# Kernel optimization log

Hardware: AMD Instinct MI355X
Metric: run time of the kernel (lower is better)

The kernel has to match this reference:

```python
import jax, jax.numpy as jnp
import numpy as np
import math

D = 1024
H = 16

def setup_inputs() -> dict:
    key = jax.random.key(0)
    ks = jax.random.split(key, 8)
    N, X, T = 2, 1024, 4096
    s = 1.0 / math.sqrt(D)
    return {
        "previous_output": jax.random.normal(ks[0], (N, X, D), jnp.float32),
        "context": jax.random.normal(ks[1], (N, T, D), jnp.float32),
        "Wq": jax.random.normal(ks[2], (D, D), jnp.float32) * s,
        "bq": jnp.zeros((D,), jnp.float32),
        "Wk": jax.random.normal(ks[3], (D, D), jnp.float32) * s,
        "bk": jnp.zeros((D,), jnp.float32),
        "Wv": jax.random.normal(ks[4], (D, D), jnp.float32) * s,
        "bv": jnp.zeros((D,), jnp.float32),
    }

def reference(previous_output, context, Wq, bq, Wk, bk, Wv, bv):
    N, X, _ = previous_output.shape
    T = context.shape[1]
    hd = D // H
    # linear projections (torch Linear: x @ W.T + b)
    q = (previous_output @ Wq.T + bq).reshape(N, X, H, hd).transpose(0, 2, 1, 3)  # (N,H,X,hd)
    k = (context @ Wk.T + bk).reshape(N, T, H, hd).transpose(0, 2, 1, 3)          # (N,H,T,hd)
    v = (context @ Wv.T + bv).reshape(N, T, H, hd).transpose(0, 2, 1, 3)          # (N,H,T,hd)
    scores = jnp.einsum('nhxd,nhtd->nhxt', q, k) / jnp.sqrt(jnp.float32(hd))       # (N,H,X,T)
    attn = jax.nn.softmax(scores, axis=-1)
    out = jnp.einsum('nhxt,nhtd->nhxd', attn, v)                                   # (N,H,X,hd)
    return out.transpose(0, 2, 1, 3).reshape(N, X, D)
```

## Files before the change

kernel.cpp:

```cpp
#include <hip/hip_runtime.h>

typedef __bf16 bf16_t;
typedef __bf16 bf16x8 __attribute__((ext_vector_type(8)));
typedef __bf16 bf16x4 __attribute__((ext_vector_type(4)));
typedef float f32x4 __attribute__((ext_vector_type(4)));

#define D_MODEL 1024
#define NHEAD 16
#define HD 64
#define XLEN 1024
#define TLEN 4096
#define NBATCH 2
#define CEXP 0.18033688011112042f

typedef __attribute__((address_space(3))) bf16_t lds_bf16;
typedef const __attribute__((address_space(1))) bf16_t glb_bf16;

#define MEMFENCE() asm volatile("" ::: "memory")

__global__ __launch_bounds__(256) void convert5(const float* __restrict__ prev, const float* __restrict__ ctx,
                                                const float* __restrict__ wq, const float* __restrict__ wk,
                                                const float* __restrict__ wv,
                                                bf16_t* __restrict__ prev_b, bf16_t* __restrict__ ctx_b,
                                                bf16_t* __restrict__ wq_b, bf16_t* __restrict__ wk_b,
                                                bf16_t* __restrict__ wv_b) {
    int b = blockIdx.x;
    const float* src; bf16_t* dst; int lb;
    if (b < 256)       { src = prev; dst = prev_b; lb = b; }
    else if (b < 1280) { src = ctx;  dst = ctx_b;  lb = b - 256; }
    else if (b < 1408) { src = wq;   dst = wq_b;   lb = b - 1280; }
    else if (b < 1536) { src = wk;   dst = wk_b;   lb = b - 1408; }
    else               { src = wv;   dst = wv_b;   lb = b - 1536; }
    const int base = lb * 8192 + threadIdx.x * 4;
#pragma unroll
    for (int i = 0; i < 8; ++i) {
        const int off = base + i * 1024;
        f32x4 f = *(const f32x4*)(src + off);
        bf16x4 h;
        h[0] = (bf16_t)f[0]; h[1] = (bf16_t)f[1]; h[2] = (bf16_t)f[2]; h[3] = (bf16_t)f[3];
        *(bf16x4*)(dst + off) = h;
    }
}

template<int MF>
__device__ __forceinline__ void gemm_core(const bf16_t* __restrict__ Xa,
                                          const bf16_t* __restrict__ Wb,
                                          int m0, int n0, char* smem,
                                          f32x4 (&acc)[MF][4]) {
    const int tid  = threadIdx.x;
    const int w    = tid >> 6;
    const int lane = tid & 63;
    const int q4   = lane >> 4;
    const int c    = lane & 15;
    const int wm   = w >> 2;
    const int wn   = w & 3;

    constexpr int ABYTES = MF * 2048;
    constexpr int BUFSZ  = ABYTES + 16384;
    constexpr int AINSTR = MF / 4;
    constexpr int NT     = 32;

#pragma unroll
    for (int i = 0; i < MF; ++i)
#pragma unroll
        for (int j = 0; j < 4; ++j) acc[i][j] = (f32x4){0.f, 0.f, 0.f, 0.f};

    const int xp = ((lane & 3) * 16) ^ (((lane >> 5) & 1) << 5);
    const char* gA = (const char*)Xa + ((size_t)(m0 + w * 16 + (lane >> 2)) << 11) + xp;
    const char* gB = (const char*)Wb + ((size_t)(n0 + w * 16 + (lane >> 2)) << 11) + xp;
    char* lw = smem + w * 1024;

    const int fo = c * 64 + ((q4 * 16) ^ (((c >> 3) & 1) << 5));

#pragma unroll
    for (int t = 0; t < 3; ++t) {
#pragma unroll
        for (int i = 0; i < AINSTR; ++i)
            __builtin_amdgcn_global_load_lds((glb_bf16*)(gA + (size_t)i * 262144 + t * 64),
                                             (lds_bf16*)(lw + t * BUFSZ + i * 8192), 16, 0, 0);
#pragma unroll
        for (int i = 0; i < 2; ++i)
            __builtin_amdgcn_global_load_lds((glb_bf16*)(gB + (size_t)i * 262144 + t * 64),
                                             (lds_bf16*)(lw + t * BUFSZ + ABYTES + i * 8192), 16, 0, 0);
        MEMFENCE();
    }

#pragma unroll 1
    for (int t = 0; t < NT; ++t) {
        if (t < NT - 2) {
            if constexpr (AINSTR == 2) asm volatile("s_waitcnt vmcnt(8)" ::: "memory");
            else                       asm volatile("s_waitcnt vmcnt(6)" ::: "memory");
        } else if (t == NT - 2) {
            if constexpr (AINSTR == 2) asm volatile("s_waitcnt vmcnt(4)" ::: "memory");
            else                       asm volatile("s_waitcnt vmcnt(3)" ::: "memory");
        } else {
            asm volatile("s_waitcnt vmcnt(0)" ::: "memory");
        }
        __builtin_amdgcn_s_barrier();
        MEMFENCE();

        const char* cbuf = smem + (t & 3) * BUFSZ;
        char* pbuf = lw + ((t + 3) & 3) * BUFSZ;
        const bool pf = (t + 3) < NT;
        const int tk = (t + 3) * 64;

        if (pf) {
#pragma unroll
            for (int i = 0; i < AINSTR; ++i)
                __builtin_amdgcn_global_load_lds((glb_bf16*)(gA + (size_t)i * 262144 + tk),
                                                 (lds_bf16*)(pbuf + i * 8192), 16, 0, 0);
        }
        bf16x8 bfrag[4];
#pragma unroll
        for (int ni = 0; ni < 4; ++ni)
            bfrag[ni] = *(const bf16x8*)(cbuf + ABYTES + (wn * 4 + ni) * 1024 + fo);
        bf16x8 afrag[MF / 2];
#pragma unroll
        for (int mi = 0; mi < MF / 2; ++mi)
            afrag[mi] = *(const bf16x8*)(cbuf + (wm * MF + mi) * 1024 + fo);
        __builtin_amdgcn_s_setprio(1);
#pragma unroll
        for (int mi = 0; mi < MF / 2; ++mi)
#pragma unroll
            for (int ni = 0; ni < 4; ++ni)
                acc[mi][ni] = __builtin_amdgcn_mfma_f32_16x16x32_bf16(afrag[mi], bfrag[ni], acc[mi][ni], 0, 0, 0);
        __builtin_amdgcn_s_setprio(0);
        MEMFENCE();
        __builtin_amdgcn_s_barrier();
        MEMFENCE();

        if (pf) {
#pragma unroll
            for (int i = 0; i < 2; ++i)
                __builtin_amdgcn_global_load_lds((glb_bf16*)(gB + (size_t)i * 262144 + tk),
                                                 (lds_bf16*)(pbuf + ABYTES + i * 8192), 16, 0, 0);
        }
        bf16x8 afrag2[MF / 2];
#pragma unroll
        for (int mi = 0; mi < MF / 2; ++mi)
            afrag2[mi] = *(const bf16x8*)(cbuf + (wm * MF + MF / 2 + mi) * 1024 + fo);
        __builtin_amdgcn_s_setprio(1);
#pragma unroll
        for (int mi = 0; mi < MF / 2; ++mi)
#pragma unroll
            for (int ni = 0; ni < 4; ++ni)
                acc[MF / 2 + mi][ni] = __builtin_amdgcn_mfma_f32_16x16x32_bf16(afrag2[mi], bfrag[ni], acc[MF / 2 + mi][ni], 0, 0, 0);
        __builtin_amdgcn_s_setprio(0);
        MEMFENCE();
    }
}

__global__ __launch_bounds__(512, 2) void gemm_fused2(
    const bf16_t* __restrict__ Xq, const bf16_t* __restrict__ Xc,
    const bf16_t* __restrict__ wq, const bf16_t* __restrict__ wk, const bf16_t* __restrict__ wv,
    const float* __restrict__ bq, const float* __restrict__ bk, const float* __restrict__ bv,
    bf16_t* __restrict__ Qh, bf16_t* __restrict__ Kh, bf16_t* __restrict__ Vt) {
    __shared__ __align__(16) char smem[131072];
    const int bid  = blockIdx.x;
    const int tid  = threadIdx.x;
    const int w    = tid >> 6;
    const int lane = tid & 63;
    const int q4   = lane >> 4;
    const int c    = lane & 15;
    const int wm   = w >> 2;
    const int wn   = w & 3;

    if (bid >= 64) {
        const int b     = bid - 64;
        const int r     = b & 7;
        const int j     = (b >> 3) & 7;
        const int mhi   = b >> 6;
        const int vmode = j >> 2;
        const int n0    = (j & 3) * 256;
        const int m0    = (mhi * 8 + r) * 256;
        const bf16_t* W   = vmode ? wv : wk;
        const float* bias = vmode ? bv : bk;

        const int Nw = n0 + wn * 64;
        float bz[4];
#pragma unroll
        for (int ni = 0; ni < 4; ++ni) bz[ni] = bias[Nw + ni * 16 + c];
        MEMFENCE();

        f32x4 acc[8][4];
        gemm_core<8>(Xc, W, m0, n0, smem, acc);

        const int Mw = m0 + wm * 128;
        const int headbase = Nw >> 6;
        if (vmode == 0) {
#pragma unroll
            for (int mi = 0; mi < 8; ++mi) {
                const int mrow = Mw + mi * 16 + q4 * 4;
                const int nb2 = mrow >> 12, pos = mrow & 4095;
                bf16_t* ob = Kh + ((size_t)(nb2 * NHEAD + headbase) * TLEN + pos) * HD;
#pragma unroll
                for (int ni = 0; ni < 4; ++ni) {
                    const int d = ni * 16 + c;
#pragma unroll
                    for (int r2 = 0; r2 < 4; ++r2)
                        ob[(size_t)r2 * HD + d] = (bf16_t)(acc[mi][ni][r2] + bz[ni]);
                }
            }
        } else {
#pragma unroll
            for (int mi = 0; mi < 8; ++mi) {
                const int mrow = Mw + mi * 16 + q4 * 4;
                const int nb2 = mrow >> 12, pos = mrow & 4095;
                const int lin = (pos & ~31) + ((pos >> 2) & 3) * 8 + ((pos >> 4) & 1) * 4;
#pragma unroll
                for (int ni = 0; ni < 4; ++ni) {
                    const int d = ni * 16 + c;
                    bf16x4 v4;
#pragma unroll
                    for (int r2 = 0; r2 < 4; ++r2) v4[r2] = (bf16_t)(acc[mi][ni][r2] + bz[ni]);
                    *(bf16x4*)(Vt + ((size_t)(nb2 * NHEAD + headbase) * HD + d) * TLEN + lin) = v4;
                }
            }
        }
    } else {
        const int b  = bid;
        const int m0 = (b >> 2) * 128;
        const int n0 = (b & 3) * 256;

        const int Nw = n0 + wn * 64;
        float bz[4];
#pragma unroll
        for (int ni = 0; ni < 4; ++ni) bz[ni] = bq[Nw + ni * 16 + c];
        MEMFENCE();

        f32x4 acc[4][4];
        gemm_core<4>(Xq, wq, m0, n0, smem, acc);

        const int Mw = m0 + wm * 64;
        const int headbase = Nw >> 6;
#pragma unroll
        for (int mi = 0; mi < 4; ++mi) {
            const int mrow = Mw + mi * 16 + q4 * 4;
            const int nb2 = mrow >> 10, pos = mrow & 1023;
            bf16_t* ob = Qh + ((size_t)(nb2 * NHEAD + headbase) * XLEN + pos) * HD;
#pragma unroll
            for (int ni = 0; ni < 4; ++ni) {
                const int d = ni * 16 + c;
#pragma unroll
                for (int r2 = 0; r2 < 4; ++r2)
                    ob[(size_t)r2 * HD + d] = (bf16_t)((acc[mi][ni][r2] + bz[ni]) * CEXP);
            }
        }
    }
}

__global__ __launch_bounds__(256, 4) void attn_kernel(const bf16_t* __restrict__ Qh,
                                                      const bf16_t* __restrict__ Kh,
                                                      const bf16_t* __restrict__ Vt,
                                                      bf16_t* __restrict__ Opart,
                                                      float* __restrict__ Lpart) {
    __shared__ __align__(16) char smem[32768];

    const int tid  = threadIdx.x;
    const int lane = tid & 63;
    const int w    = tid >> 6;
    const int q4   = lane >> 4;
    const int c    = lane & 15;

    const int bid = blockIdx.x;
    const int xcd = bid & 7;
    const int seq = bid >> 3;
    const int tq  = seq & 3;
    const int xb  = (seq >> 2) & 7;
    const int g   = seq >> 5;
    const int nh  = g * 8 + xcd;
    const int xw  = xb * 128 + w * 32;

    const bf16_t* __restrict__ Kb = Kh + (size_t)nh * TLEN * HD;
    const bf16_t* __restrict__ Vb = Vt + (size_t)nh * HD * TLEN;

    bf16x8 qa[2][2];
#pragma unroll
    for (int mi = 0; mi < 2; ++mi) {
        const bf16_t* qr = Qh + ((size_t)nh * XLEN + xw + mi * 16 + c) * HD + q4 * 8;
        qa[mi][0] = *(const bf16x8*)(qr);
        qa[mi][1] = *(const bf16x8*)(qr + 32);
    }

    const int sRow0 = tid >> 3,  sRow1 = 32 + (tid >> 3);
    const int sCh   = tid & 7;
    const int kCol0 = ((sCh ^ (sRow0 & 7)) * 8);
    const int kCol1 = ((sCh ^ (sRow1 & 7)) * 8);

    const int ofs0 = c * 128 + ((q4 ^ (c & 7)) * 16);
    const int ofs1 = c * 128 + (((4 + q4) ^ (c & 7)) * 16);

    f32x4 o[2][4];
#pragma unroll
    for (int i = 0; i < 2; ++i)
#pragma unroll
        for (int j = 0; j < 4; ++j) o[i][j] = (f32x4){0.f, 0.f, 0.f, 0.f};
    f32x4 lacc[2];
    lacc[0] = (f32x4){0.f, 0.f, 0.f, 0.f};
    lacc[1] = (f32x4){0.f, 0.f, 0.f, 0.f};

    bf16x8 ones8;
#pragma unroll
    for (int j = 0; j < 8; ++j) ones8[j] = (bf16_t)1.0f;

    const int t0base = tq * (TLEN / 4);

    {
        bf16_t* base = (bf16_t*)smem;
        __builtin_amdgcn_global_load_lds((glb_bf16*)(Kb + (size_t)(t0base + sRow0) * HD + kCol0), (lds_bf16*)(base + w * 512), 16, 0, 0);
        __builtin_amdgcn_global_load_lds((glb_bf16*)(Kb + (size_t)(t0base + sRow1) * HD + kCol1), (lds_bf16*)(base + 2048 + w * 512), 16, 0, 0);
        __builtin_amdgcn_global_load_lds((glb_bf16*)(Vb + (size_t)sRow0 * TLEN + t0base + kCol0), (lds_bf16*)(base + 4096 + w * 512), 16, 0, 0);
        __builtin_amdgcn_global_load_lds((glb_bf16*)(Vb + (size_t)sRow1 * TLEN + t0base + kCol1), (lds_bf16*)(base + 6144 + w * 512), 16, 0, 0);
    }

    for (int s = 0; s < 16; ++s) {
        __syncthreads();
        if (s < 15) {
            const int t1 = t0base + (s + 1) * 64;
            bf16_t* base = (bf16_t*)smem + ((s + 1) & 1) * 8192;
            __builtin_amdgcn_global_load_lds((glb_bf16*)(Kb + (size_t)(t1 + sRow0) * HD + kCol0), (lds_bf16*)(base + w * 512), 16, 0, 0);
            __builtin_amdgcn_global_load_lds((glb_bf16*)(Kb + (size_t)(t1 + sRow1) * HD + kCol1), (lds_bf16*)(base + 2048 + w * 512), 16, 0, 0);
            __builtin_amdgcn_global_load_lds((glb_bf16*)(Vb + (size_t)sRow0 * TLEN + t1 + kCol0), (lds_bf16*)(base + 4096 + w * 512), 16, 0, 0);
            __builtin_amdgcn_global_load_lds((glb_bf16*)(Vb + (size_t)sRow1 * TLEN + t1 + kCol1), (lds_bf16*)(base + 6144 + w * 512), 16, 0, 0);
        }

        const char* KtB = smem + (s & 1) * 16384;
        const char* VsB = KtB + 8192;
#pragma unroll
        for (int g32 = 0; g32 < 2; ++g32) {
            bf16x8 p8[2];
#pragma unroll
            for (int tt = 0; tt < 2; ++tt) {
                const int rofs = g32 * 4096 + tt * 2048;
                bf16x8 kb0 = *(const bf16x8*)(KtB + rofs + ofs0);
                bf16x8 kb1 = *(const bf16x8*)(KtB + rofs + ofs1);
#pragma unroll
                for (int mi = 0; mi < 2; ++mi) {
                    f32x4 sv = (f32x4){0.f, 0.f, 0.f, 0.f};
                    sv = __builtin_amdgcn_mfma_f32_16x16x32_bf16(kb0, qa[mi][0], sv, 0, 0, 0);
                    sv = __builtin_amdgcn_mfma_f32_16x16x32_bf16(kb1, qa[mi][1], sv, 0, 0, 0);
#pragma unroll
                    for (int r = 0; r < 4; ++r)
                        p8[mi][tt * 4 + r] = (bf16_t)__builtin_exp2f(sv[r]);
                }
            }
            const int vsel = g32 ? ofs1 : ofs0;
            bf16x8 va[4];
#pragma unroll
            for (int dt = 0; dt < 4; ++dt)
                va[dt] = *(const bf16x8*)(VsB + vsel + dt * 2048);
#pragma unroll
            for (int mi = 0; mi < 2; ++mi) {
#pragma unroll
                for (int dt = 0; dt < 4; ++dt)
                    o[mi][dt] = __builtin_amdgcn_mfma_f32_16x16x32_bf16(va[dt], p8[mi], o[mi][dt], 0, 0, 0);
                lacc[mi] = __builtin_amdgcn_mfma_f32_16x16x32_bf16(ones8, p8[mi], lacc[mi], 0, 0, 0);
            }
        }
    }

    __syncthreads();
    bf16_t* Ob = (bf16_t*)smem;
    float*  Lb = (float*)(smem + 16896);
#pragma unroll
    for (int mi = 0; mi < 2; ++mi) {
        if (q4 == 0) Lb[w * 32 + mi * 16 + c] = lacc[mi][0];
#pragma unroll
        for (int dt = 0; dt < 4; ++dt)
#pragma unroll
            for (int r = 0; r < 4; ++r)
                Ob[w * 2112 + (dt * 16 + q4 * 4 + r) * 33 + mi * 16 + c] = (bf16_t)o[mi][dt][r];
    }
    {
        const int lr = lane >> 1;
        const int dh = lane & 1;
        bf16x8 out4[4];
#pragma unroll
        for (int j2 = 0; j2 < 4; ++j2)
#pragma unroll
            for (int e = 0; e < 8; ++e)
                out4[j2][e] = Ob[w * 2112 + (dh * 32 + j2 * 8 + e) * 33 + lr];
        const size_t pair = (size_t)nh * XLEN + xw + lr;
        bf16_t* op = Opart + (pair * 4 + tq) * HD + dh * 32;
#pragma unroll
        for (int j2 = 0; j2 < 4; ++j2)
            *(bf16x8*)(op + j2 * 8) = out4[j2];
        if (dh == 0) Lpart[pair * 4 + tq] = Lb[w * 32 + lr];
    }
}

__global__ __launch_bounds__(256) void attn_merge(const bf16_t* __restrict__ Opart,
                                                  const float* __restrict__ Lpart,
                                                  float* __restrict__ Out) {
    const int u    = blockIdx.x * 256 + threadIdx.x;
    const int pair = u >> 3;
    const int d0   = (u & 7) * 8;
    const int nh   = pair >> 10;
    const int x    = pair & 1023;
    const int n    = nh >> 4;
    const int h    = nh & 15;

    float l = 0.f;
    float s[8];
#pragma unroll
    for (int j = 0; j < 8; ++j) s[j] = 0.f;
#pragma unroll
    for (int tqi = 0; tqi < 4; ++tqi) {
        l += Lpart[pair * 4 + tqi];
        bf16x8 v = *(const bf16x8*)(Opart + ((size_t)pair * 4 + tqi) * HD + d0);
#pragma unroll
        for (int j = 0; j < 8; ++j) s[j] += (float)v[j];
    }
    const float inv = 1.0f / l;
    f32x4 v0, v1;
#pragma unroll
    for (int j = 0; j < 4; ++j) { v0[j] = s[j] * inv; v1[j] = s[4 + j] * inv; }
    float* op = Out + ((size_t)(n * XLEN + x)) * D_MODEL + h * HD + d0;
    *(f32x4*)(op)     = v0;
    *(f32x4*)(op + 4) = v1;
}

extern "C" void kernel_launch(void* const* d_in, const int* in_sizes, int n_in,
                              void* d_out, int out_size, void* d_ws, size_t ws_size,
                              hipStream_t stream) {
    (void)in_sizes; (void)n_in; (void)out_size; (void)ws_size;
    const float* prev = (const float*)d_in[0];
    const float* ctx  = (const float*)d_in[1];
    const float* Wq   = (const float*)d_in[2];
    const float* bq   = (const float*)d_in[3];
    const float* Wk   = (const float*)d_in[4];
    const float* bk   = (const float*)d_in[5];
    const float* Wv   = (const float*)d_in[6];
    const float* bv   = (const float*)d_in[7];

    const size_t MiB = 1024 * 1024;
    char* ws = (char*)d_ws;
    bf16_t* prev_b = (bf16_t*)(ws);
    bf16_t* ctx_b  = (bf16_t*)(ws + 4 * MiB);
    bf16_t* wq_b   = (bf16_t*)(ws + 20 * MiB);
    bf16_t* wk_b   = (bf16_t*)(ws + 22 * MiB);
    bf16_t* wv_b   = (bf16_t*)(ws + 24 * MiB);
    bf16_t* Qh     = (bf16_t*)(ws + 26 * MiB);
    bf16_t* Kh     = (bf16_t*)(ws + 30 * MiB);
    bf16_t* Vt     = (bf16_t*)(ws + 46 * MiB);
    bf16_t* Opart  = ctx_b;
    float*  Lpart  = (float*)prev_b;

    convert5<<<1664, 256, 0, stream>>>(prev, ctx, Wq, Wk, Wv, prev_b, ctx_b, wq_b, wk_b, wv_b);
    gemm_fused2<<<320, 512, 0, stream>>>(prev_b, ctx_b, wq_b, wk_b, wv_b, bq, bk, bv, Qh, Kh, Vt);
    attn_kernel<<<1024, 256, 0, stream>>>(Qh, Kh, Vt, Opart, Lpart);
    attn_merge<<<1024, 256, 0, stream>>>(Opart, Lpart, (float*)d_out);
}
```

Measured before the change: 202.9 us.

## Move deep LDS prefetch ring from GEMM to attention, halve T-split

The projection GEMM drops its 4-stage, 3-ahead global-to-LDS ring for a 2-buffer scheme with a full vmcnt(0) wait each step. Its LDS shrinks to 64 KiB and its launch bound rises to 4 blocks per SM. The attention kernel goes the other way: it gains a 4-buffer, 3-ahead prefetch ring with partial vmcnt waits and setprio around its MFMAs. It also splits T into 2 chunks instead of 4, giving 512 blocks and fewer partials for the merge kernel to combine. The risks are GEMM latency exposure from the full waits, lower attention occupancy with 64 KiB LDS, and fewer attention blocks to fill the GPU.

```diff
diff --git a/kernel.cpp b/kernel.cpp
--- a/kernel.cpp
+++ b/kernel.cpp
@@ -73,68 +73,52 @@
     const int fo = c * 64 + ((q4 * 16) ^ (((c >> 3) & 1) << 5));
 
 #pragma unroll
-    for (int t = 0; t < 3; ++t) {
-#pragma unroll
-        for (int i = 0; i < AINSTR; ++i)
-            __builtin_amdgcn_global_load_lds((glb_bf16*)(gA + (size_t)i * 262144 + t * 64),
-                                             (lds_bf16*)(lw + t * BUFSZ + i * 8192), 16, 0, 0);
-#pragma unroll
-        for (int i = 0; i < 2; ++i)
-            __builtin_amdgcn_global_load_lds((glb_bf16*)(gB + (size_t)i * 262144 + t * 64),
-                                             (lds_bf16*)(lw + t * BUFSZ + ABYTES + i * 8192), 16, 0, 0);
-        MEMFENCE();
-    }
+    for (int i = 0; i < AINSTR; ++i)
+        __builtin_amdgcn_global_load_lds((glb_bf16*)(gA + (size_t)i * 262144),
+                                         (lds_bf16*)(lw + i * 8192), 16, 0, 0);
+#pragma unroll
+    for (int i = 0; i < 2; ++i)
+        __builtin_amdgcn_global_load_lds((glb_bf16*)(gB + (size_t)i * 262144),
+                                         (lds_bf16*)(lw + ABYTES + i * 8192), 16, 0, 0);
+    MEMFENCE();
 
 #pragma unroll 1
     for (int t = 0; t < NT; ++t) {
-        if (t < NT - 2) {
-            if constexpr (AINSTR == 2) asm volatile("s_waitcnt vmcnt(8)" ::: "memory");
-            else                       asm volatile("s_waitcnt vmcnt(6)" ::: "memory");
-        } else if (t == NT - 2) {
-            if constexpr (AINSTR == 2) asm volatile("s_waitcnt vmcnt(4)" ::: "memory");
-            else                       asm volatile("s_waitcnt vmcnt(3)" ::: "memory");
-        } else {
-            asm volatile("s_waitcnt vmcnt(0)" ::: "memory");
-        }
+        asm volatile("s_waitcnt vmcnt(0)" ::: "memory");
         __builtin_amdgcn_s_barrier();
         MEMFENCE();
 
-        const char* cbuf = smem + (t & 3) * BUFSZ;
-        char* pbuf = lw + ((t + 3) & 3) * BUFSZ;
-        const bool pf = (t + 3) < NT;
-        const int tk = (t + 3) * 64;
-
-        if (pf) {
+        if (t + 1 < NT) {
+            char* pbuf = lw + ((t + 1) & 1) * BUFSZ;
+            const int tk = (t + 1) * 64;
 #pragma unroll
             for (int i = 0; i < AINSTR; ++i)
                 __builtin_amdgcn_global_load_lds((glb_bf16*)(gA + (size_t)i * 262144 + tk),
                                                  (lds_bf16*)(pbuf + i * 8192), 16, 0, 0);
-        }
-        bf16x8 bfrag[4];
-#pragma unroll
-        for (int ni = 0; ni < 4; ++ni)
-            bfrag[ni] = *(const bf16x8*)(cbuf + ABYTES + (wn * 4 + ni) * 1024 + fo);
-        bf16x8 afrag[MF / 2];
-#pragma unroll
-        for (int mi = 0; mi < MF / 2; ++mi)
-            afrag[mi] = *(const bf16x8*)(cbuf + (wm * MF + mi) * 1024 + fo);
-        __builtin_amdgcn_s_setprio(1);
-#pragma unroll
-        for (int mi = 0; mi < MF / 2; ++mi)
-#pragma unroll
-            for (int ni = 0; ni < 4; ++ni)
-                acc[mi][ni] = __builtin_amdgcn_mfma_f32_16x16x32_bf16(afrag[mi], bfrag[ni], acc[mi][ni], 0, 0, 0);
-        __builtin_amdgcn_s_setprio(0);
-        MEMFENCE();
-        __builtin_amdgcn_s_barrier();
-        MEMFENCE();
-
-        if (pf) {
 #pragma unroll
             for (int i = 0; i < 2; ++i)
                 __builtin_amdgcn_global_load_lds((glb_bf16*)(gB + (size_t)i * 262144 + tk),
                                                  (lds_bf16*)(pbuf + ABYTES + i * 8192), 16, 0, 0);
         }
+
+        const char* cbuf = smem + (t & 1) * BUFSZ;
+
+        bf16x8 bfrag[4];
+#pragma unroll
+        for (int ni = 0; ni < 4; ++ni)
+            bfrag[ni] = *(const bf16x8*)(cbuf + ABYTES + (wn * 4 + ni) * 1024 + fo);
+        bf16x8 afrag[MF / 2];
+#pragma unroll
+        for (int mi = 0; mi < MF / 2; ++mi)
+            afrag[mi] = *(const bf16x8*)(cbuf + (wm * MF + mi) * 1024 + fo);
+        __builtin_amdgcn_s_setprio(1);
+#pragma unroll
+        for (int mi = 0; mi < MF / 2; ++mi)
+#pragma unroll
+            for (int ni = 0; ni < 4; ++ni)
+                acc[mi][ni] = __builtin_amdgcn_mfma_f32_16x16x32_bf16(afrag[mi], bfrag[ni], acc[mi][ni], 0, 0, 0);
+        __builtin_amdgcn_s_setprio(0);
+
         bf16x8 afrag2[MF / 2];
 #pragma unroll
         for (int mi = 0; mi < MF / 2; ++mi)
@@ -150,12 +134,12 @@
     }
 }
 
-__global__ __launch_bounds__(512, 2) void gemm_fused2(
+__global__ __launch_bounds__(512, 4) void gemm_fused2(
     const bf16_t* __restrict__ Xq, const bf16_t* __restrict__ Xc,
     const bf16_t* __restrict__ wq, const bf16_t* __restrict__ wk, const bf16_t* __restrict__ wv,
     const float* __restrict__ bq, const float* __restrict__ bk, const float* __restrict__ bv,
     bf16_t* __restrict__ Qh, bf16_t* __restrict__ Kh, bf16_t* __restrict__ Vt) {
-    __shared__ __align__(16) char smem[131072];
+    __shared__ __align__(16) char smem[65536];
     const int bid  = blockIdx.x;
     const int tid  = threadIdx.x;
     const int w    = tid >> 6;
@@ -164,6 +148,7 @@
     const int c    = lane & 15;
     const int wm   = w >> 2;
     const int wn   = w & 3;
+    (void)w;
 
     if (bid >= 64) {
         const int b     = bid - 64;
@@ -249,12 +234,12 @@
     }
 }
 
-__global__ __launch_bounds__(256, 4) void attn_kernel(const bf16_t* __restrict__ Qh,
+__global__ __launch_bounds__(256, 2) void attn_kernel(const bf16_t* __restrict__ Qh,
                                                       const bf16_t* __restrict__ Kh,
                                                       const bf16_t* __restrict__ Vt,
                                                       bf16_t* __restrict__ Opart,
                                                       float* __restrict__ Lpart) {
-    __shared__ __align__(16) char smem[32768];
+    __shared__ __align__(16) char smem[65536];
 
     const int tid  = threadIdx.x;
     const int lane = tid & 63;
@@ -265,9 +250,9 @@
     const int bid = blockIdx.x;
     const int xcd = bid & 7;
     const int seq = bid >> 3;
-    const int tq  = seq & 3;
-    const int xb  = (seq >> 2) & 7;
-    const int g   = seq >> 5;
+    const int tq  = seq & 1;
+    const int xb  = (seq >> 1) & 7;
+    const int g   = seq >> 4;
     const int nh  = g * 8 + xcd;
     const int xw  = xb * 128 + w * 32;
 
@@ -303,28 +288,38 @@
 #pragma unroll
     for (int j = 0; j < 8; ++j) ones8[j] = (bf16_t)1.0f;
 
-    const int t0base = tq * (TLEN / 4);
-
-    {
-        bf16_t* base = (bf16_t*)smem;
-        __builtin_amdgcn_global_load_lds((glb_bf16*)(Kb + (size_t)(t0base + sRow0) * HD + kCol0), (lds_bf16*)(base + w * 512), 16, 0, 0);
-        __builtin_amdgcn_global_load_lds((glb_bf16*)(Kb + (size_t)(t0base + sRow1) * HD + kCol1), (lds_bf16*)(base + 2048 + w * 512), 16, 0, 0);
-        __builtin_amdgcn_global_load_lds((glb_bf16*)(Vb + (size_t)sRow0 * TLEN + t0base + kCol0), (lds_bf16*)(base + 4096 + w * 512), 16, 0, 0);
-        __builtin_amdgcn_global_load_lds((glb_bf16*)(Vb + (size_t)sRow1 * TLEN + t0base + kCol1), (lds_bf16*)(base + 6144 + w * 512), 16, 0, 0);
-    }
-
-    for (int s = 0; s < 16; ++s) {
-        __syncthreads();
-        if (s < 15) {
-            const int t1 = t0base + (s + 1) * 64;
-            bf16_t* base = (bf16_t*)smem + ((s + 1) & 1) * 8192;
+    const int t0base = tq * (TLEN / 2);
+    const int NS = 32;
+
+#pragma unroll
+    for (int s = 0; s < 3; ++s) {
+        const int t1 = t0base + s * 64;
+        bf16_t* base = (bf16_t*)smem + s * 8192;
+        __builtin_amdgcn_global_load_lds((glb_bf16*)(Kb + (size_t)(t1 + sRow0) * HD + kCol0), (lds_bf16*)(base + w * 512), 16, 0, 0);
+        __builtin_amdgcn_global_load_lds((glb_bf16*)(Kb + (size_t)(t1 + sRow1) * HD + kCol1), (lds_bf16*)(base + 2048 + w * 512), 16, 0, 0);
+        __builtin_amdgcn_global_load_lds((glb_bf16*)(Vb + (size_t)sRow0 * TLEN + t1 + kCol0), (lds_bf16*)(base + 4096 + w * 512), 16, 0, 0);
+        __builtin_amdgcn_global_load_lds((glb_bf16*)(Vb + (size_t)sRow1 * TLEN + t1 + kCol1), (lds_bf16*)(base + 6144 + w * 512), 16, 0, 0);
+        MEMFENCE();
+    }
+
+#pragma unroll 1
+    for (int s = 0; s < NS; ++s) {
+        if (s < NS - 2)      asm volatile("s_waitcnt vmcnt(8)" ::: "memory");
+        else if (s == NS - 2) asm volatile("s_waitcnt vmcnt(4)" ::: "memory");
+        else                  asm volatile("s_waitcnt vmcnt(0)" ::: "memory");
+        __builtin_amdgcn_s_barrier();
+        MEMFENCE();
+
+        if (s + 3 < NS) {
+            const int t1 = t0base + (s + 3) * 64;
+            bf16_t* base = (bf16_t*)smem + ((s + 3) & 3) * 8192;
             __builtin_amdgcn_global_load_lds((glb_bf16*)(Kb + (size_t)(t1 + sRow0) * HD + kCol0), (lds_bf16*)(base + w * 512), 16, 0, 0);
             __builtin_amdgcn_global_load_lds((glb_bf16*)(Kb + (size_t)(t1 + sRow1) * HD + kCol1), (lds_bf16*)(base + 2048 + w * 512), 16, 0, 0);
             __builtin_amdgcn_global_load_lds((glb_bf16*)(Vb + (size_t)sRow0 * TLEN + t1 + kCol0), (lds_bf16*)(base + 4096 + w * 512), 16, 0, 0);
             __builtin_amdgcn_global_load_lds((glb_bf16*)(Vb + (size_t)sRow1 * TLEN + t1 + kCol1), (lds_bf16*)(base + 6144 + w * 512), 16, 0, 0);
         }
 
-        const char* KtB = smem + (s & 1) * 16384;
+        const char* KtB = smem + (s & 3) * 16384;
         const char* VsB = KtB + 8192;
 #pragma unroll
         for (int g32 = 0; g32 < 2; ++g32) {
@@ -349,6 +344,7 @@
 #pragma unroll
             for (int dt = 0; dt < 4; ++dt)
                 va[dt] = *(const bf16x8*)(VsB + vsel + dt * 2048);
+            __builtin_amdgcn_s_setprio(1);
 #pragma unroll
             for (int mi = 0; mi < 2; ++mi) {
 #pragma unroll
@@ -356,7 +352,9 @@
                     o[mi][dt] = __builtin_amdgcn_mfma_f32_16x16x32_bf16(va[dt], p8[mi], o[mi][dt], 0, 0, 0);
                 lacc[mi] = __builtin_amdgcn_mfma_f32_16x16x32_bf16(ones8, p8[mi], lacc[mi], 0, 0, 0);
             }
+            __builtin_amdgcn_s_setprio(0);
         }
+        MEMFENCE();
     }
 
     __syncthreads();
@@ -381,11 +379,11 @@
             for (int e = 0; e < 8; ++e)
                 out4[j2][e] = Ob[w * 2112 + (dh * 32 + j2 * 8 + e) * 33 + lr];
         const size_t pair = (size_t)nh * XLEN + xw + lr;
-        bf16_t* op = Opart + (pair * 4 + tq) * HD + dh * 32;
+        bf16_t* op = Opart + (pair * 2 + tq) * HD + dh * 32;
 #pragma unroll
         for (int j2 = 0; j2 < 4; ++j2)
             *(bf16x8*)(op + j2 * 8) = out4[j2];
-        if (dh == 0) Lpart[pair * 4 + tq] = Lb[w * 32 + lr];
+        if (dh == 0) Lpart[pair * 2 + tq] = Lb[w * 32 + lr];
     }
 }
 
@@ -405,9 +403,9 @@
 #pragma unroll
     for (int j = 0; j < 8; ++j) s[j] = 0.f;
 #pragma unroll
-    for (int tqi = 0; tqi < 4; ++tqi) {
-        l += Lpart[pair * 4 + tqi];
-        bf16x8 v = *(const bf16x8*)(Opart + ((size_t)pair * 4 + tqi) * HD + d0);
+    for (int tqi = 0; tqi < 2; ++tqi) {
+        l += Lpart[pair * 2 + tqi];
+        bf16x8 v = *(const bf16x8*)(Opart + ((size_t)pair * 2 + tqi) * HD + d0);
 #pragma unroll
         for (int j = 0; j < 8; ++j) s[j] += (float)v[j];
     }
@@ -448,6 +446,6 @@
 
     convert5<<<1664, 256, 0, stream>>>(prev, ctx, Wq, Wk, Wv, prev_b, ctx_b, wq_b, wk_b, wv_b);
     gemm_fused2<<<320, 512, 0, stream>>>(prev_b, ctx_b, wq_b, wk_b, wv_b, bq, bk, bv, Qh, Kh, Vt);
-    attn_kernel<<<1024, 256, 0, stream>>>(Qh, Kh, Vt, Opart, Lpart);
+    attn_kernel<<<512, 256, 0, stream>>>(Qh, Kh, Vt, Opart, Lpart);
     attn_merge<<<1024, 256, 0, stream>>>(Opart, Lpart, (float*)d_out);
 }
```

Result: slower. 356.0 us (+75.4%).

## Switch projection GEMM to double-buffered 128-wide K tiles

Applied to the files above, without the earlier changes.

The projection GEMM core now uses two LDS buffers, each holding a 128-wide K slice, instead of four buffers with 64-wide slices prefetched three stages ahead. This halves the iteration count and drops one barrier per K step. In exchange, each iteration waits for all outstanding loads (vmcnt(0)) and prefetches only one tile ahead, so global load latency is less hidden. Total LDS footprint is unchanged.

```diff
diff --git a/kernel.cpp b/kernel.cpp
--- a/kernel.cpp
+++ b/kernel.cpp
@@ -55,10 +55,10 @@
     const int wm   = w >> 2;
     const int wn   = w & 3;
 
-    constexpr int ABYTES = MF * 2048;
-    constexpr int BUFSZ  = ABYTES + 16384;
-    constexpr int AINSTR = MF / 4;
-    constexpr int NT     = 32;
+    constexpr int ABYTES = MF * 4096;
+    constexpr int BUFSZ  = ABYTES + 32768;
+    constexpr int AI     = MF / 4;
+    constexpr int NT     = 16;
 
 #pragma unroll
     for (int i = 0; i < MF; ++i)
@@ -73,80 +73,74 @@
     const int fo = c * 64 + ((q4 * 16) ^ (((c >> 3) & 1) << 5));
 
 #pragma unroll
-    for (int t = 0; t < 3; ++t) {
-#pragma unroll
-        for (int i = 0; i < AINSTR; ++i)
-            __builtin_amdgcn_global_load_lds((glb_bf16*)(gA + (size_t)i * 262144 + t * 64),
-                                             (lds_bf16*)(lw + t * BUFSZ + i * 8192), 16, 0, 0);
-#pragma unroll
-        for (int i = 0; i < 2; ++i)
-            __builtin_amdgcn_global_load_lds((glb_bf16*)(gB + (size_t)i * 262144 + t * 64),
-                                             (lds_bf16*)(lw + t * BUFSZ + ABYTES + i * 8192), 16, 0, 0);
-        MEMFENCE();
-    }
+    for (int i = 0; i < AI; ++i)
+#pragma unroll
+        for (int k = 0; k < 2; ++k)
+            __builtin_amdgcn_global_load_lds((glb_bf16*)(gA + (size_t)i * 262144 + k * 64),
+                                             (lds_bf16*)(lw + k * (MF * 2048) + i * 8192), 16, 0, 0);
+#pragma unroll
+    for (int i = 0; i < 2; ++i)
+#pragma unroll
+        for (int k = 0; k < 2; ++k)
+            __builtin_amdgcn_global_load_lds((glb_bf16*)(gB + (size_t)i * 262144 + k * 64),
+                                             (lds_bf16*)(lw + ABYTES + k * 16384 + i * 8192), 16, 0, 0);
+    MEMFENCE();
 
 #pragma unroll 1
     for (int t = 0; t < NT; ++t) {
-        if (t < NT - 2) {
-            if constexpr (AINSTR == 2) asm volatile("s_waitcnt vmcnt(8)" ::: "memory");
-            else                       asm volatile("s_waitcnt vmcnt(6)" ::: "memory");
-        } else if (t == NT - 2) {
-            if constexpr (AINSTR == 2) asm volatile("s_waitcnt vmcnt(4)" ::: "memory");
-            else                       asm volatile("s_waitcnt vmcnt(3)" ::: "memory");
-        } else {
-            asm volatile("s_waitcnt vmcnt(0)" ::: "memory");
-        }
+        asm volatile("s_waitcnt vmcnt(0)" ::: "memory");
         __builtin_amdgcn_s_barrier();
         MEMFENCE();
 
-        const char* cbuf = smem + (t & 3) * BUFSZ;
-        char* pbuf = lw + ((t + 3) & 3) * BUFSZ;
-        const bool pf = (t + 3) < NT;
-        const int tk = (t + 3) * 64;
-
-        if (pf) {
-#pragma unroll
-            for (int i = 0; i < AINSTR; ++i)
-                __builtin_amdgcn_global_load_lds((glb_bf16*)(gA + (size_t)i * 262144 + tk),
-                                                 (lds_bf16*)(pbuf + i * 8192), 16, 0, 0);
-        }
-        bf16x8 bfrag[4];
-#pragma unroll
-        for (int ni = 0; ni < 4; ++ni)
-            bfrag[ni] = *(const bf16x8*)(cbuf + ABYTES + (wn * 4 + ni) * 1024 + fo);
-        bf16x8 afrag[MF / 2];
-#pragma unroll
-        for (int mi = 0; mi < MF / 2; ++mi)
-            afrag[mi] = *(const bf16x8*)(cbuf + (wm * MF + mi) * 1024 + fo);
-        __builtin_amdgcn_s_setprio(1);
-#pragma unroll
-        for (int mi = 0; mi < MF / 2; ++mi)
+        if (t + 1 < NT) {
+            char* pb = lw + ((t + 1) & 1) * BUFSZ;
+            const size_t tk = (size_t)(t + 1) * 128;
+#pragma unroll
+            for (int i = 0; i < AI; ++i)
+#pragma unroll
+                for (int k = 0; k < 2; ++k)
+                    __builtin_amdgcn_global_load_lds((glb_bf16*)(gA + (size_t)i * 262144 + tk + k * 64),
+                                                     (lds_bf16*)(pb + k * (MF * 2048) + i * 8192), 16, 0, 0);
+#pragma unroll
+            for (int i = 0; i < 2; ++i)
+#pragma unroll
+                for (int k = 0; k < 2; ++k)
+                    __builtin_amdgcn_global_load_lds((glb_bf16*)(gB + (size_t)i * 262144 + tk + k * 64),
+                                                     (lds_bf16*)(pb + ABYTES + k * 16384 + i * 8192), 16, 0, 0);
+        }
+
+        const char* cb = smem + (t & 1) * BUFSZ;
+#pragma unroll
+        for (int kk = 0; kk < 2; ++kk) {
+            bf16x8 bfrag[4];
 #pragma unroll
             for (int ni = 0; ni < 4; ++ni)
-                acc[mi][ni] = __builtin_amdgcn_mfma_f32_16x16x32_bf16(afrag[mi], bfrag[ni], acc[mi][ni], 0, 0, 0);
-        __builtin_amdgcn_s_setprio(0);
-        MEMFENCE();
-        __builtin_amdgcn_s_barrier();
-        MEMFENCE();
-
-        if (pf) {
-#pragma unroll
-            for (int i = 0; i < 2; ++i)
-                __builtin_amdgcn_global_load_lds((glb_bf16*)(gB + (size_t)i * 262144 + tk),
-                                                 (lds_bf16*)(pbuf + ABYTES + i * 8192), 16, 0, 0);
-        }
-        bf16x8 afrag2[MF / 2];
-#pragma unroll
-        for (int mi = 0; mi < MF / 2; ++mi)
-            afrag2[mi] = *(const bf16x8*)(cbuf + (wm * MF + MF / 2 + mi) * 1024 + fo);
-        __builtin_amdgcn_s_setprio(1);
-#pragma unroll
-        for (int mi = 0; mi < MF / 2; ++mi)
-#pragma unroll
-            for (int ni = 0; ni < 4; ++ni)
-                acc[MF / 2 + mi][ni] = __builtin_amdgcn_mfma_f32_16x16x32_bf16(afrag2[mi], bfrag[ni], acc[MF / 2 + mi][ni], 0, 0, 0);
-        __builtin_amdgcn_s_setprio(0);
-        MEMFENCE();
+                bfrag[ni] = *(const bf16x8*)(cb + ABYTES + kk * 16384 + (wn * 4 + ni) * 1024 + fo);
+            bf16x8 afrag[MF / 2];
+#pragma unroll
+            for (int mi = 0; mi < MF / 2; ++mi)
+                afrag[mi] = *(const bf16x8*)(cb + kk * (MF * 2048) + (wm * MF + mi) * 1024 + fo);
+            __builtin_amdgcn_s_setprio(1);
+#pragma unroll
+            for (int mi = 0; mi < MF / 2; ++mi)
+#pragma unroll
+                for (int ni = 0; ni < 4; ++ni)
+                    acc[mi][ni] = __builtin_amdgcn_mfma_f32_16x16x32_bf16(afrag[mi], bfrag[ni], acc[mi][ni], 0, 0, 0);
+            __builtin_amdgcn_s_setprio(0);
+
+            bf16x8 afrag2[MF / 2];
+#pragma unroll
+            for (int mi = 0; mi < MF / 2; ++mi)
+                afrag2[mi] = *(const bf16x8*)(cb + kk * (MF * 2048) + (wm * MF + MF / 2 + mi) * 1024 + fo);
+            __builtin_amdgcn_s_setprio(1);
+#pragma unroll
+            for (int mi = 0; mi < MF / 2; ++mi)
+#pragma unroll
+                for (int ni = 0; ni < 4; ++ni)
+                    acc[MF / 2 + mi][ni] = __builtin_amdgcn_mfma_f32_16x16x32_bf16(afrag2[mi], bfrag[ni], acc[MF / 2 + mi][ni], 0, 0, 0);
+            __builtin_amdgcn_s_setprio(0);
+            MEMFENCE();
+        }
     }
 }
 
@@ -164,6 +158,7 @@
     const int c    = lane & 15;
     const int wm   = w >> 2;
     const int wn   = w & 3;
+    (void)w;
 
     if (bid >= 64) {
         const int b     = bid - 64;
```

Result: no change. 202.1 us (-0.4%).
